# Kernel optimization log

Hardware: AMD Instinct MI355X
Metric: run time of the kernel (lower is better)

The kernel has to match this reference:

```python
import jax, jax.numpy as jnp
import numpy as np

ALPHA = 0.9  # init alpha, adj='DAD'


def setup_inputs() -> dict:
    key = jax.random.key(0)
    k1, k2, k3, k4 = jax.random.split(key, 4)
    N, C, E = 100000, 64, 3200000
    labels = jax.random.uniform(k1, (N, C), dtype=jnp.float32)
    mask = jax.random.randint(k2, (N,), 0, 2).astype(bool)
    src = jax.random.randint(k3, (E,), 0, N, dtype=jnp.int64)
    dst = jax.random.randint(k4, (E,), 0, N, dtype=jnp.int64)
    return {"labels": labels, "mask": mask, "src": src, "dst": dst, "num_layers": 10}


def reference(labels, mask, src, dst, num_layers):
    N = labels.shape[0]
    # mask: y = zeros; y[mask] = labels[mask]
    y0 = jnp.where(mask[:, None], labels, jnp.zeros((), labels.dtype))
    last = (1.0 - ALPHA) * y0  # confidence = 1
    # in-degrees via scatter-count at dst, clamped to >= 1
    degs = jax.ops.segment_sum(jnp.ones(dst.shape, labels.dtype), dst, num_segments=N)
    degs = jnp.maximum(degs, 1.0)
    norm = (degs ** -0.5)[:, None]  # DAD: D^-1/2 on both sides

    def step(y, _):
        y = norm * y                                   # left D^-1/2
        h = jax.ops.segment_sum(y[src], dst, num_segments=N)  # A @ y (copy_u + sum)
        y = ALPHA * h * norm                           # right D^-1/2
        y = jnp.clip(last + y, 0.0, 1.0)               # post_step clamp
        return y, None

    y, _ = jax.lax.scan(step, y0, None, length=num_layers)
    return y
```

## Files before the change

kernel.cpp:

```cpp
#include <hip/hip_runtime.h>
#include <hip/hip_fp16.h>


#define ALPHA 0.9f
#define C 64
#define BSHIFT 9
#define NCHUNK 256

typedef float f32x4 __attribute__((ext_vector_type(4)));
typedef unsigned int u32;
typedef unsigned int u32x2 __attribute__((ext_vector_type(2)));


__global__ void chunk_hist_kernel(const int* __restrict__ dst, int* __restrict__ cnt,
                                  int E, int epc) {
    __shared__ int h[256];
    h[threadIdx.x] = 0;
    __syncthreads();
    int c = blockIdx.x;
    int e1 = min(c * epc + epc, E);
    for (int e = c * epc + threadIdx.x; e < e1; e += 256) {
        int d = __builtin_nontemporal_load(&dst[e]);
        atomicAdd(&h[d >> BSHIFT], 1);
    }
    __syncthreads();
    cnt[c * 256 + threadIdx.x] = h[threadIdx.x];
}

__global__ void bucket_scan_kernel(int* __restrict__ cnt, int* __restrict__ bucket_base,
                                   int* __restrict__ row_ptr, int N, int E) {
    __shared__ int tmp[256];
    int b = threadIdx.x;
    int s = 0;
    for (int c = 0; c < NCHUNK; ++c) {
        int t = cnt[c * 256 + b];
        cnt[c * 256 + b] = s;
        s += t;
    }
    tmp[b] = s;
    __syncthreads();
    int v = s;
    for (int off = 1; off < 256; off <<= 1) {
        int add = (b >= off) ? tmp[b - off] : 0;
        __syncthreads();
        tmp[b] += add;
        __syncthreads();
    }
    bucket_base[b] = tmp[b] - v;
    if (b == 255) { bucket_base[256] = tmp[255]; row_ptr[N] = E; }
}

__global__ void bucket_scatter_kernel(const int* __restrict__ src, const int* __restrict__ dst,
                                      const int* __restrict__ cnt,
                                      const int* __restrict__ bucket_base,
                                      unsigned* __restrict__ tmp, int E, int epc) {
    __shared__ int cur[256];
    int c = blockIdx.x;
    cur[threadIdx.x] = bucket_base[threadIdx.x] + cnt[c * 256 + threadIdx.x];
    __syncthreads();
    int e1 = min(c * epc + epc, E);
    for (int e = c * epc + threadIdx.x; e < e1; e += 256) {
        int d = __builtin_nontemporal_load(&dst[e]);
        int s = __builtin_nontemporal_load(&src[e]);
        int pos = atomicAdd(&cur[d >> BSHIFT], 1);
        tmp[pos] = ((unsigned)(d & 511) << 23) | (unsigned)s;
    }
}

__global__ void bucket_sort_kernel(const unsigned* __restrict__ tmp,
                                   const int* __restrict__ bucket_base,
                                   int* __restrict__ row_ptr,
                                   float* __restrict__ norm,
                                   int* __restrict__ col, int N) {
    __shared__ int ldeg[512];
    __shared__ int lexc[512];
    __shared__ int lcur[512];
    __shared__ int stmp[256];
    int b = blockIdx.x;
    int lo = b << BSHIFT;
    int nn = min(512, N - lo);
    int ebeg = bucket_base[b];
    int eend = bucket_base[b + 1];
    int t = threadIdx.x;
    ldeg[t] = 0; ldeg[t + 256] = 0;
    __syncthreads();
    for (int e = ebeg + t; e < eend; e += 256) {
        atomicAdd(&ldeg[tmp[e] >> 23], 1);
    }
    __syncthreads();
    int d0 = ldeg[2 * t], d1 = ldeg[2 * t + 1];
    int p = d0 + d1;
    stmp[t] = p;
    __syncthreads();
    for (int off = 1; off < 256; off <<= 1) {
        int add = (t >= off) ? stmp[t - off] : 0;
        __syncthreads();
        stmp[t] += add;
        __syncthreads();
    }
    int excp = stmp[t] - p;
    lexc[2 * t] = excp;
    lexc[2 * t + 1] = excp + d0;
    __syncthreads();
    for (int i = t; i < nn; i += 256) {
        int rp = ebeg + lexc[i];
        row_ptr[lo + i] = rp;
        lcur[i] = rp;
        norm[lo + i] = rsqrtf(fmaxf((float)ldeg[i], 1.0f));
    }
    __syncthreads();
    for (int e = ebeg + t; e < eend; e += 256) {
        unsigned pk = tmp[e];
        int pos = atomicAdd(&lcur[pk >> 23], 1);
        col[pos] = (int)(pk & 0x7FFFFFu);
    }
}

__global__ void pack_col_kernel(int* __restrict__ col, const float* __restrict__ norm,
                                int E) {
    int i = blockIdx.x * blockDim.x + threadIdx.x;
    if (i >= E) return;
    u32 s = (u32)col[i];
    u32 nq = (u32)(norm[s] * 32767.0f + 0.5f);
    col[i] = (int)(s | (nq << 17));
}


__global__ void init_z8_kernel(const float* __restrict__ labels,
                               const int* __restrict__ mask,
                               unsigned char* __restrict__ z8,
                               unsigned char* __restrict__ last8,
                               int total8 ) {
    int i = blockIdx.x * blockDim.x + threadIdx.x;
    if (i >= total8) return;
    int node = i >> 3;
    int g = i & 7;
    const float* lrow = labels + (size_t)node * C + g * 8;
    f32x4 a  = __builtin_nontemporal_load((const f32x4*)lrow);
    f32x4 bv = __builtin_nontemporal_load((const f32x4*)lrow + 1);
    bool mk = mask[node] != 0;
    float v[8] = {a.x, a.y, a.z, a.w, bv.x, bv.y, bv.z, bv.w};
    float m = mk ? 255.0f : 0.0f;
    u32 q0 = 0, q1 = 0;
#pragma unroll
    for (int k = 0; k < 4; ++k) q0 |= ((u32)(v[k] * m + 0.5f)) << (8 * k);
#pragma unroll
    for (int k = 0; k < 4; ++k) q1 |= ((u32)(v[k + 4] * m + 0.5f)) << (8 * k);
    u32x2 qq; qq.x = q0; qq.y = q1;
    ((u32x2*)(z8 + (size_t)node * C))[g] = qq;
    ((u32x2*)(last8 + (size_t)node * C))[g] = qq;
}


template <bool OUT_FP32>
__global__ void prop_kernel(const unsigned char* __restrict__ z8_old,
                            unsigned char* __restrict__ z8_new,
                            void* __restrict__ out_f32,
                            const int* __restrict__ row_ptr,
                            const int* __restrict__ col,
                            const float* __restrict__ norm,
                            const unsigned char* __restrict__ last8, int N) {
    int gtid = blockIdx.x * blockDim.x + threadIdx.x;
    int wid = gtid >> 6;
    int lane = threadIdx.x & 63;
    int node = (wid << 1) + (lane >> 5);
    int sub = (lane >> 3) & 3;
    int ch8 = lane & 7;

    bool ok = node < N;
    int beg = 0, end = 0;
    if (ok) { beg = row_ptr[node]; end = row_ptr[node + 1]; }
    int deg = end - beg;
    int lastc = max(end - 1, 0);
    int Tl = (deg + 3) >> 2;
    int T = max(Tl, __shfl_xor(Tl, 32, 64));

    const float DQ = 1.0f / (32767.0f * 255.0f);

    float acc[8];
#pragma unroll
    for (int k = 0; k < 8; ++k) acc[k] = 0.0f;

    if (T > 0) {
        int base = beg + sub;

        float n0, n1, n2, n3, n4, n5, n6, n7;
        uint2 r0, r1, r2, r3, r4, r5, r6, r7;

#define FETCH(t, nv, rv)                                                      \
        do {                                                                  \
            int pp = base + ((t) << 2);                                       \
            int pcl = min(pp, lastc);                                         \
            u32 pk = (u32)col[pcl];                                           \
            int sv = (int)(pk & 0x1FFFFu);                                    \
            float sc = (float)(pk >> 17) * DQ;                                \
            nv = (pp < end) ? sc : 0.0f;                                      \
            rv = ((const uint2*)(z8_old + (size_t)sv * C))[ch8];              \
        } while (0)

#define CONSUME(nv, rv)                                                       \
        do {                                                                  \
            u32 q0 = rv.x, q1 = rv.y;                                         \
            acc[0] = fmaf((float)(q0 & 0xffu),         nv, acc[0]);           \
            acc[1] = fmaf((float)((q0 >> 8) & 0xffu),  nv, acc[1]);           \
            acc[2] = fmaf((float)((q0 >> 16) & 0xffu), nv, acc[2]);           \
            acc[3] = fmaf((float)(q0 >> 24),           nv, acc[3]);           \
            acc[4] = fmaf((float)(q1 & 0xffu),         nv, acc[4]);           \
            acc[5] = fmaf((float)((q1 >> 8) & 0xffu),  nv, acc[5]);           \
            acc[6] = fmaf((float)((q1 >> 16) & 0xffu), nv, acc[6]);           \
            acc[7] = fmaf((float)(q1 >> 24),           nv, acc[7]);           \
        } while (0)

        FETCH(0, n0, r0); FETCH(1, n1, r1); FETCH(2, n2, r2); FETCH(3, n3, r3);
        FETCH(4, n4, r4); FETCH(5, n5, r5); FETCH(6, n6, r6); FETCH(7, n7, r7);
        int t = 8;
        for (; t + 8 <= T; t += 8) {
            CONSUME(n0, r0); FETCH(t + 0, n0, r0);
            CONSUME(n1, r1); FETCH(t + 1, n1, r1);
            CONSUME(n2, r2); FETCH(t + 2, n2, r2);
            CONSUME(n3, r3); FETCH(t + 3, n3, r3);
            CONSUME(n4, r4); FETCH(t + 4, n4, r4);
            CONSUME(n5, r5); FETCH(t + 5, n5, r5);
            CONSUME(n6, r6); FETCH(t + 6, n6, r6);
            CONSUME(n7, r7); FETCH(t + 7, n7, r7);
        }
        int rr = T - t;
        if (rr > 0) { CONSUME(n0, r0); FETCH(t + 0, n0, r0); }
        if (rr > 1) { CONSUME(n1, r1); FETCH(t + 1, n1, r1); }
        if (rr > 2) { CONSUME(n2, r2); FETCH(t + 2, n2, r2); }
        if (rr > 3) { CONSUME(n3, r3); FETCH(t + 3, n3, r3); }
        if (rr > 4) { CONSUME(n4, r4); FETCH(t + 4, n4, r4); }
        if (rr > 5) { CONSUME(n5, r5); FETCH(t + 5, n5, r5); }
        if (rr > 6) { CONSUME(n6, r6); FETCH(t + 6, n6, r6); }
        CONSUME(n0, r0); CONSUME(n1, r1); CONSUME(n2, r2); CONSUME(n3, r3);
        CONSUME(n4, r4); CONSUME(n5, r5); CONSUME(n6, r6); CONSUME(n7, r7);
#undef FETCH
#undef CONSUME
    }

#pragma unroll
    for (int k = 0; k < 8; ++k) {
        acc[k] += __shfl_xor(acc[k], 8, 64);
        acc[k] += __shfl_xor(acc[k], 16, 64);
    }

    if (sub == 0 && ok) {
        float nr = norm[node];
        float anr = ALPHA * nr;
        const float LC = (1.0f - ALPHA) / 255.0f;
        uint2 lq = ((const uint2*)(last8 + (size_t)node * C))[ch8];
        u32 l0 = lq.x, l1 = lq.y;
        float la[8];
        la[0] = (float)(l0 & 0xffu) * LC;
        la[1] = (float)((l0 >> 8) & 0xffu) * LC;
        la[2] = (float)((l0 >> 16) & 0xffu) * LC;
        la[3] = (float)(l0 >> 24) * LC;
        la[4] = (float)(l1 & 0xffu) * LC;
        la[5] = (float)((l1 >> 8) & 0xffu) * LC;
        la[6] = (float)((l1 >> 16) & 0xffu) * LC;
        la[7] = (float)(l1 >> 24) * LC;
        float o[8];
#pragma unroll
        for (int k = 0; k < 8; ++k)
            o[k] = fminf(fmaxf(fmaf(anr, acc[k], la[k]), 0.0f), 1.0f);
        if (OUT_FP32) {
            float* orow = (float*)out_f32 + (size_t)node * C + ch8 * 8;
            float4 v0; v0.x = o[0]; v0.y = o[1]; v0.z = o[2]; v0.w = o[3];
            float4 v1; v1.x = o[4]; v1.y = o[5]; v1.z = o[6]; v1.w = o[7];
            ((float4*)orow)[0] = v0;
            ((float4*)orow)[1] = v1;
        } else {
            u32 q0 = 0, q1 = 0;
#pragma unroll
            for (int k = 0; k < 4; ++k) q0 |= ((u32)(o[k] * 255.0f + 0.5f)) << (8 * k);
#pragma unroll
            for (int k = 0; k < 4; ++k) q1 |= ((u32)(o[k + 4] * 255.0f + 0.5f)) << (8 * k);
            uint2 qq; qq.x = q0; qq.y = q1;
            ((uint2*)(z8_new + (size_t)node * C))[ch8] = qq;
        }
    }
}


__global__ void zero_f32_kernel(float* __restrict__ p, int n) {
    int i = blockIdx.x * blockDim.x + threadIdx.x;
    if (i < n) p[i] = 0.0f;
}
__global__ void deg_count_f_kernel(const int* __restrict__ dst, float* __restrict__ deg, int E) {
    int i = blockIdx.x * blockDim.x + threadIdx.x;
    if (i < E) atomicAdd(&deg[dst[i]], 1.0f);
}
__global__ void make_norm_f_kernel(float* __restrict__ deg, int N) {
    int i = blockIdx.x * blockDim.x + threadIdx.x;
    if (i < N) deg[i] = rsqrtf(fmaxf(deg[i], 1.0f));
}
__global__ void init_yh_kernel(const float* __restrict__ labels, const int* __restrict__ mask,
                               float* __restrict__ y, float* __restrict__ h, int total4) {
    int i = blockIdx.x * blockDim.x + threadIdx.x;
    if (i >= total4) return;
    int row = i >> 4;
    float4 lv = ((const float4*)labels)[i];
    float m = (mask[row] != 0) ? 1.0f : 0.0f;
    float4 yv; yv.x = m * lv.x; yv.y = m * lv.y; yv.z = m * lv.z; yv.w = m * lv.w;
    ((float4*)y)[i] = yv;
    float4 z; z.x = 0.f; z.y = 0.f; z.z = 0.f; z.w = 0.f;
    ((float4*)h)[i] = z;
}
__global__ void scatter_kernel(const float* __restrict__ y, const int* __restrict__ src,
                               const int* __restrict__ dst, const float* __restrict__ norm,
                               float* __restrict__ h, int E) {
    int gtid = blockIdx.x * blockDim.x + threadIdx.x;
    int e = gtid >> 6;
    int lane = threadIdx.x & 63;
    if (e >= E) return;
    int s = src[e]; int d = dst[e];
    float v = y[(size_t)s * C + lane] * norm[s];
    atomicAdd(&h[(size_t)d * C + lane], v);
}
__global__ void finalize_kernel(const float* __restrict__ labels, const int* __restrict__ mask,
                                const float* __restrict__ norm, float* __restrict__ h,
                                float* __restrict__ y, int total4) {
    int i = blockIdx.x * blockDim.x + threadIdx.x;
    if (i >= total4) return;
    int row = i >> 4;
    float4 hv = ((float4*)h)[i];
    float4 lv = ((const float4*)labels)[i];
    float m = (mask[row] != 0) ? (1.0f - ALPHA) : 0.0f;
    float nr = norm[row];
    float4 o;
    o.x = fminf(fmaxf(m * lv.x + ALPHA * hv.x * nr, 0.0f), 1.0f);
    o.y = fminf(fmaxf(m * lv.y + ALPHA * hv.y * nr, 0.0f), 1.0f);
    o.z = fminf(fmaxf(m * lv.z + ALPHA * hv.z * nr, 0.0f), 1.0f);
    o.w = fminf(fmaxf(m * lv.w + ALPHA * hv.w * nr, 0.0f), 1.0f);
    ((float4*)y)[i] = o;
    float4 z; z.x = 0.f; z.y = 0.f; z.z = 0.f; z.w = 0.f;
    ((float4*)h)[i] = z;
}


extern "C" void kernel_launch(void* const* d_in, const int* in_sizes, int n_in,
                              void* d_out, int out_size, void* d_ws, size_t ws_size,
                              hipStream_t stream) {
    const float* labels = (const float*)d_in[0];
    const int*   mask   = (const int*)d_in[1];
    const int*   src    = (const int*)d_in[2];
    const int*   dst    = (const int*)d_in[3];

    const int N = in_sizes[1];
    const int E = in_sizes[2];
    const int num_layers = 10;
    const int B = 256;

    size_t fixed_ints = (size_t)257 + (size_t)NCHUNK * 256 + (N + 1) + N + E;
    size_t z8bytes = (size_t)N * C;
    size_t tmpbytes = (size_t)E * 4;
    size_t span = (tmpbytes > 2 * z8bytes ? tmpbytes : 2 * z8bytes);
    size_t need = fixed_ints * 4 + 256 + span + z8bytes;
    bool pack_ok = (N < (1 << 17));

    if (ws_size >= need && pack_ok) {
        char* w = (char*)d_ws;
        int*   bucket_base = (int*)w;             w += 257 * 4;
        int*   cnt         = (int*)w;             w += (size_t)NCHUNK * 256 * 4;
        int*   row_ptr     = (int*)w;             w += (size_t)(N + 1) * 4;
        float* norm        = (float*)w;           w += (size_t)N * 4;
        int*   col         = (int*)w;             w += (size_t)E * 4;
        w = (char*)(((uintptr_t)w + 255) & ~(uintptr_t)255);
        unsigned char* z8A = (unsigned char*)w;
        unsigned char* z8B = z8A + z8bytes;
        unsigned* tmp      = (unsigned*)z8A;
        w += span;
        unsigned char* last8 = (unsigned char*)w;

        int epc = (E + NCHUNK - 1) / NCHUNK;
        int NB = (N + 511) >> BSHIFT;

        chunk_hist_kernel<<<NCHUNK, 256, 0, stream>>>(dst, cnt, E, epc);
        bucket_scan_kernel<<<1, 256, 0, stream>>>(cnt, bucket_base, row_ptr, N, E);
        bucket_scatter_kernel<<<NCHUNK, 256, 0, stream>>>(src, dst, cnt, bucket_base,
                                                          tmp, E, epc);
        bucket_sort_kernel<<<NB, 256, 0, stream>>>(tmp, bucket_base, row_ptr,
                                                   norm, col, N);
        pack_col_kernel<<<(E + B - 1) / B, B, 0, stream>>>(col, norm, E);

        int total8 = N * 8;
        init_z8_kernel<<<(total8 + B - 1) / B, B, 0, stream>>>(labels, mask,
                                                               z8A, last8, total8);
        const int nwaves = (N + 1) >> 1;
        const int prop_blocks = (int)(((size_t)nwaves * 64 + B - 1) / B);
        for (int l = 0; l < num_layers - 1; ++l) {
            unsigned char* zi = (l & 1) ? z8B : z8A;
            unsigned char* zo = (l & 1) ? z8A : z8B;
            prop_kernel<false><<<prop_blocks, B, 0, stream>>>(zi, zo, nullptr,
                                                              row_ptr, col, norm,
                                                              last8, N);
        }
        prop_kernel<true><<<prop_blocks, B, 0, stream>>>(z8B, nullptr, d_out,
                                                         row_ptr, col, norm,
                                                         last8, N);
    } else {
        const int total4 = N * C / 4;
        float* y = (float*)d_out;
        float* wsf = (float*)d_ws;
        float* norm = wsf;
        float* h = wsf + ((N + 15) & ~15);
        zero_f32_kernel<<<(N + B - 1) / B, B, 0, stream>>>(norm, N);
        deg_count_f_kernel<<<(E + B - 1) / B, B, 0, stream>>>(dst, norm, E);
        make_norm_f_kernel<<<(N + B - 1) / B, B, 0, stream>>>(norm, N);
        init_yh_kernel<<<(total4 + B - 1) / B, B, 0, stream>>>(labels, mask, y, h, total4);
        const int scatter_blocks = (int)(((size_t)E * C + B - 1) / B);
        for (int l = 0; l < num_layers; ++l) {
            scatter_kernel<<<scatter_blocks, B, 0, stream>>>(y, src, dst, norm, h, E);
            finalize_kernel<<<(total4 + B - 1) / B, B, 0, stream>>>(labels, mask, norm,
                                                                    h, y, total4);
        }
    }
}
```

Before: 647.7 us.

## Use finer 128-node buckets and parallelize chunk-offset scan across buckets

Shrinks CSR-build buckets from 512 to 128 destination nodes, giving about 782 buckets instead of about 196 so the bucket_sort kernel launches more blocks and each block does a smaller scan. The old single-block serial scan over 256 chunks is replaced by a per-bucket parallel chunk scan plus a 1024-wide base scan, and the count array is stored bucket-major. In exchange there is one extra kernel launch, larger shared histograms with more zeroing, and half of each 256-thread sort block sits idle in the scan.

```diff
diff --git a/kernel.cpp b/kernel.cpp
--- a/kernel.cpp
+++ b/kernel.cpp
@@ -4,7 +4,8 @@
 
 #define ALPHA 0.9f
 #define C 64
-#define BSHIFT 9
+#define BSHIFT 7
+#define MAXB 1024
 #define NCHUNK 256
 
 typedef float f32x4 __attribute__((ext_vector_type(4)));
@@ -14,8 +15,8 @@
 
 __global__ void chunk_hist_kernel(const int* __restrict__ dst, int* __restrict__ cnt,
                                   int E, int epc) {
-    __shared__ int h[256];
-    h[threadIdx.x] = 0;
+    __shared__ int h[MAXB];
+    for (int i = threadIdx.x; i < MAXB; i += 256) h[i] = 0;
     __syncthreads();
     int c = blockIdx.x;
     int e1 = min(c * epc + epc, E);
@@ -24,46 +25,59 @@
         atomicAdd(&h[d >> BSHIFT], 1);
     }
     __syncthreads();
-    cnt[c * 256 + threadIdx.x] = h[threadIdx.x];
-}
-
-__global__ void bucket_scan_kernel(int* __restrict__ cnt, int* __restrict__ bucket_base,
-                                   int* __restrict__ row_ptr, int N, int E) {
-    __shared__ int tmp[256];
-    int b = threadIdx.x;
-    int s = 0;
-    for (int c = 0; c < NCHUNK; ++c) {
-        int t = cnt[c * 256 + b];
-        cnt[c * 256 + b] = s;
-        s += t;
-    }
-    tmp[b] = s;
-    __syncthreads();
-    int v = s;
+    for (int i = threadIdx.x; i < MAXB; i += 256) cnt[i * NCHUNK + c] = h[i];
+}
+
+__global__ void chunk_scan_kernel(int* __restrict__ cnt, int* __restrict__ bucket_tot) {
+    __shared__ int v[256];
+    int b = blockIdx.x;
+    int t = threadIdx.x;
+    int x = cnt[b * NCHUNK + t];
+    v[t] = x;
+    __syncthreads();
     for (int off = 1; off < 256; off <<= 1) {
-        int add = (b >= off) ? tmp[b - off] : 0;
-        __syncthreads();
-        tmp[b] += add;
-        __syncthreads();
-    }
-    bucket_base[b] = tmp[b] - v;
-    if (b == 255) { bucket_base[256] = tmp[255]; row_ptr[N] = E; }
+        int add = (t >= off) ? v[t - off] : 0;
+        __syncthreads();
+        v[t] += add;
+        __syncthreads();
+    }
+    cnt[b * NCHUNK + t] = v[t] - x;
+    if (t == 255) bucket_tot[b] = v[255];
+}
+
+__global__ void base_scan_kernel(const int* __restrict__ bucket_tot,
+                                 int* __restrict__ bucket_base,
+                                 int* __restrict__ row_ptr, int N, int E, int nb) {
+    __shared__ int v[MAXB];
+    int t = threadIdx.x;
+    int x = (t < nb) ? bucket_tot[t] : 0;
+    v[t] = x;
+    __syncthreads();
+    for (int off = 1; off < MAXB; off <<= 1) {
+        int add = (t >= off) ? v[t - off] : 0;
+        __syncthreads();
+        v[t] += add;
+        __syncthreads();
+    }
+    bucket_base[t] = v[t] - x;
+    if (t == MAXB - 1) { bucket_base[MAXB] = v[MAXB - 1]; row_ptr[N] = E; }
 }
 
 __global__ void bucket_scatter_kernel(const int* __restrict__ src, const int* __restrict__ dst,
                                       const int* __restrict__ cnt,
                                       const int* __restrict__ bucket_base,
                                       unsigned* __restrict__ tmp, int E, int epc) {
-    __shared__ int cur[256];
+    __shared__ int cur[MAXB];
     int c = blockIdx.x;
-    cur[threadIdx.x] = bucket_base[threadIdx.x] + cnt[c * 256 + threadIdx.x];
+    for (int i = threadIdx.x; i < MAXB; i += 256)
+        cur[i] = bucket_base[i] + cnt[i * NCHUNK + c];
     __syncthreads();
     int e1 = min(c * epc + epc, E);
     for (int e = c * epc + threadIdx.x; e < e1; e += 256) {
         int d = __builtin_nontemporal_load(&dst[e]);
         int s = __builtin_nontemporal_load(&src[e]);
         int pos = atomicAdd(&cur[d >> BSHIFT], 1);
-        tmp[pos] = ((unsigned)(d & 511) << 23) | (unsigned)s;
+        tmp[pos] = ((unsigned)(d & 127) << 24) | (unsigned)s;
     }
 }
 
@@ -72,47 +86,40 @@
                                    int* __restrict__ row_ptr,
                                    float* __restrict__ norm,
                                    int* __restrict__ col, int N) {
-    __shared__ int ldeg[512];
-    __shared__ int lexc[512];
-    __shared__ int lcur[512];
-    __shared__ int stmp[256];
+    __shared__ int ldeg[128];
+    __shared__ int lexc[128];
+    __shared__ int lcur[128];
     int b = blockIdx.x;
     int lo = b << BSHIFT;
-    int nn = min(512, N - lo);
+    int nn = min(128, N - lo);
     int ebeg = bucket_base[b];
     int eend = bucket_base[b + 1];
     int t = threadIdx.x;
-    ldeg[t] = 0; ldeg[t + 256] = 0;
+    if (t < 128) ldeg[t] = 0;
     __syncthreads();
     for (int e = ebeg + t; e < eend; e += 256) {
-        atomicAdd(&ldeg[tmp[e] >> 23], 1);
-    }
-    __syncthreads();
-    int d0 = ldeg[2 * t], d1 = ldeg[2 * t + 1];
-    int p = d0 + d1;
-    stmp[t] = p;
-    __syncthreads();
-    for (int off = 1; off < 256; off <<= 1) {
-        int add = (t >= off) ? stmp[t - off] : 0;
-        __syncthreads();
-        stmp[t] += add;
-        __syncthreads();
-    }
-    int excp = stmp[t] - p;
-    lexc[2 * t] = excp;
-    lexc[2 * t + 1] = excp + d0;
-    __syncthreads();
-    for (int i = t; i < nn; i += 256) {
-        int rp = ebeg + lexc[i];
-        row_ptr[lo + i] = rp;
-        lcur[i] = rp;
-        norm[lo + i] = rsqrtf(fmaxf((float)ldeg[i], 1.0f));
+        atomicAdd(&ldeg[tmp[e] >> 24], 1);
+    }
+    __syncthreads();
+    if (t < 128) lexc[t] = ldeg[t];
+    __syncthreads();
+    for (int off = 1; off < 128; off <<= 1) {
+        int add = (t >= off && t < 128) ? lexc[t - off] : 0;
+        __syncthreads();
+        if (t < 128) lexc[t] += add;
+        __syncthreads();
+    }
+    if (t < nn) {
+        int rp = ebeg + lexc[t] - ldeg[t];
+        row_ptr[lo + t] = rp;
+        lcur[t] = rp;
+        norm[lo + t] = rsqrtf(fmaxf((float)ldeg[t], 1.0f));
     }
     __syncthreads();
     for (int e = ebeg + t; e < eend; e += 256) {
         unsigned pk = tmp[e];
-        int pos = atomicAdd(&lcur[pk >> 23], 1);
-        col[pos] = (int)(pk & 0x7FFFFFu);
+        int pos = atomicAdd(&lcur[pk >> 24], 1);
+        col[pos] = (int)(pk & 0xFFFFFFu);
     }
 }
 
@@ -351,7 +358,8 @@
     const int num_layers = 10;
     const int B = 256;
 
-    size_t fixed_ints = (size_t)257 + (size_t)NCHUNK * 256 + (N + 1) + N + E;
+    size_t fixed_ints = (size_t)(MAXB + 1) + MAXB + (size_t)NCHUNK * MAXB
+                      + (N + 1) + N + E;
     size_t z8bytes = (size_t)N * C;
     size_t tmpbytes = (size_t)E * 4;
     size_t span = (tmpbytes > 2 * z8bytes ? tmpbytes : 2 * z8bytes);
@@ -360,8 +368,9 @@
 
     if (ws_size >= need && pack_ok) {
         char* w = (char*)d_ws;
-        int*   bucket_base = (int*)w;             w += 257 * 4;
-        int*   cnt         = (int*)w;             w += (size_t)NCHUNK * 256 * 4;
+        int*   bucket_base = (int*)w;             w += (size_t)(MAXB + 1) * 4;
+        int*   bucket_tot  = (int*)w;             w += (size_t)MAXB * 4;
+        int*   cnt         = (int*)w;             w += (size_t)NCHUNK * MAXB * 4;
         int*   row_ptr     = (int*)w;             w += (size_t)(N + 1) * 4;
         float* norm        = (float*)w;           w += (size_t)N * 4;
         int*   col         = (int*)w;             w += (size_t)E * 4;
@@ -373,13 +382,15 @@
         unsigned char* last8 = (unsigned char*)w;
 
         int epc = (E + NCHUNK - 1) / NCHUNK;
-        int NB = (N + 511) >> BSHIFT;
+        int nb = (N + (1 << BSHIFT) - 1) >> BSHIFT;
 
         chunk_hist_kernel<<<NCHUNK, 256, 0, stream>>>(dst, cnt, E, epc);
-        bucket_scan_kernel<<<1, 256, 0, stream>>>(cnt, bucket_base, row_ptr, N, E);
+        chunk_scan_kernel<<<nb, 256, 0, stream>>>(cnt, bucket_tot);
+        base_scan_kernel<<<1, MAXB, 0, stream>>>(bucket_tot, bucket_base,
+                                                 row_ptr, N, E, nb);
         bucket_scatter_kernel<<<NCHUNK, 256, 0, stream>>>(src, dst, cnt, bucket_base,
                                                           tmp, E, epc);
-        bucket_sort_kernel<<<NB, 256, 0, stream>>>(tmp, bucket_base, row_ptr,
+        bucket_sort_kernel<<<nb, 256, 0, stream>>>(tmp, bucket_base, row_ptr,
                                                    norm, col, N);
         pack_col_kernel<<<(E + B - 1) / B, B, 0, stream>>>(col, norm, E);
 
```

After: 650.2 us. Within noise of the previous version (+0.4%).
